# Optimization experiments

Hardware: AMD Instinct MI355X
Metric: run time of the kernel (lower is better)

Reference implementation:

```python
import jax, jax.numpy as jnp
import numpy as np

A0, A1, A2 = 1.0, 1.0, 0.5  # Taylor coefficients of exp around 0 (p=2)

B, H, N, D = 2, 16, 4096, 32


def setup_inputs() -> dict:
    key = jax.random.key(0)
    kq, kk, kv = jax.random.split(key, 3)
    q = jax.random.normal(kq, (B, H, N, D), dtype=jnp.float32)
    k = jax.random.normal(kk, (B, H, N, D), dtype=jnp.float32)
    v = jax.random.normal(kv, (B, H, N, D), dtype=jnp.float32)
    return {"q": q, "k": k, "v": v}


def reference(q, k, v):
    # fastmax_function with p=2, mask=False, normalize=False, dropout=0 -> temperature=1
    b, h, n, d = q.shape
    # quadratic feature maps: flatten of outer products, [b,h,n,d*d]
    q2 = (q[..., :, None] * q[..., None, :]).reshape(b, h, n, d * d)
    k2 = (k[..., :, None] * k[..., None, :]).reshape(b, h, n, d * d)
    # numerator: a0*sum(v) + a1*q(k^T v) + a2*q2(k2^T v)
    second_term = A1 * jnp.einsum('bhnd,bhne->bhde', k, v)           # [b,h,d,d]
    third_term = A2 * jnp.einsum('bhnf,bhne->bhfe', k2, v)           # [b,h,d^2,d]
    ans = (jnp.einsum('bhnd,bhde->bhne', q, second_term)
           + jnp.einsum('bhnf,bhfe->bhne', q2, third_term)
           + A0 * jnp.sum(v, axis=-2, keepdims=True))                 # [b,h,n,d]
    # denominator: a0*n + a1*q.sum(k) + a2*q2.sum(k2)
    div = (A0 * n
           + A1 * jnp.einsum('bhnd,bhd->bhn', q, jnp.sum(k, axis=-2))
           + A2 * jnp.einsum('bhnf,bhf->bhn', q2, jnp.sum(k2, axis=-2)))  # [b,h,n]
    return ans / div[..., None]
```

## Files before the change

### kernel.cpp

```cpp
#include <hip/hip_runtime.h>

#define NTOK 4096
#define NBH  32
#define NF   576
#define NE   33
#define NKT  18
#define GTF_BH (NKT * 3 * 64 * 8)
#define GTF_HALF (9 * 3 * 64 * 8)
#define KC   16
#define NSTG 2
#define NVB  (KC * NBH)
#define NP8  (NBH * NE * NF / 8)

typedef _Float16 half_t;
typedef _Float16 half8 __attribute__((ext_vector_type(8)));
typedef _Float16 half4v __attribute__((ext_vector_type(4)));
typedef float f32x4 __attribute__((ext_vector_type(4)));
typedef unsigned int u32;

#define MFMA16(A,B,C) __builtin_amdgcn_mfma_f32_16x16x32_f16((A),(B),(C),0,0,0)

#define ASYNC_CP16(dst_lds, src_glb) \
    __builtin_amdgcn_global_load_lds( \
        (const __attribute__((address_space(1))) u32*)(const void*)(src_glb), \
        (__attribute__((address_space(3))) u32*)(void*)(dst_lds), 16, 0, 0)

static __device__ __forceinline__ half8 splat8(half_t x) {
    return (half8){x, x, x, x, x, x, x, x};
}

static __device__ __forceinline__ int FS(int d) { return (d + (d >> 3)) & 15; }

__global__ __launch_bounds__(256, 2)
void ta_kernel(const float* __restrict__ kin, const float* __restrict__ vin,
               half_t* __restrict__ P)
{
    __shared__ __align__(16) half_t kb0[2 * 4096];
    __shared__ __align__(16) half_t vb0[2 * 4096];

    const int vb = blockIdx.x;
    const int bh = vb & (NBH - 1), kc = vb >> 5;
    const int t = threadIdx.x;
    const int w = t >> 6, lane = t & 63, l16 = lane & 15, quad = lane >> 4;
    const int pw = w * 144;
    const half8 h05 = splat8((half_t)0.5f);

    f32x4 acc[9][3];
    #pragma unroll
    for (int m = 0; m < 9; ++m)
        #pragma unroll
        for (int e = 0; e < 3; ++e)
            acc[m][e] = (f32x4){0.f, 0.f, 0.f, 0.f};

    int rotoff[9], rotsalt[9];
    #pragma unroll
    for (int mt = 0; mt < 9; ++mt) {
        const int pm = pw + mt * 16;
        int ro = 0, rs = 0;
        if (pm >= 32 && pm < 512) {
            const int s  = 1 + ((pm - 32) >> 5);
            const int i0 = (pm - 32) & 31;
            const int r  = (i0 + l16 + s) & 31;
            ro = r * 128;
            rs = FS(r);
        }
        rotoff[mt] = ro;
        rotsalt[mt] = rs;
    }
    const int sh0 = FS(l16), sh1 = FS(l16 + 16);

    const size_t fbase = ((size_t)bh * NTOK + kc * 256) * 32;
    const float4* k4 = (const float4*)kin + fbase / 4;
    const float4* v4 = (const float4*)vin + fbase / 4;

    float kaf[16], vaf[16];
    auto loadst = [&](int s) {
        const int base = s * 1024;
        #pragma unroll
        for (int r = 0; r < 4; ++r) {
            float4 kk = k4[base + t + 256 * r];
            float4 vv = v4[base + t + 256 * r];
            kaf[4*r+0] = kk.x; kaf[4*r+1] = kk.y; kaf[4*r+2] = kk.z; kaf[4*r+3] = kk.w;
            vaf[4*r+0] = vv.x; vaf[4*r+1] = vv.y; vaf[4*r+2] = vv.z; vaf[4*r+3] = vv.w;
        }
    };
    auto writest = [&](int buf) {
        half_t* kb = kb0 + buf * 4096;
        half_t* vb2 = vb0 + buf * 4096;
        #pragma unroll
        for (int r = 0; r < 4; ++r) {
            const int fi = t + 256 * r;
            const int n = fi >> 3, d4 = fi & 7;
            const int c = n >> 3, j = n & 7;
            #pragma unroll
            for (int i = 0; i < 4; ++i) {
                const int d = 4 * d4 + i;
                const int a = d * 128 + ((c ^ FS(d)) << 3) + j;
                kb[a] = (half_t)kaf[4*r+i];
                vb2[a] = (half_t)vaf[4*r+i];
            }
        }
    };
    auto compute = [&](int buf) {
        const half_t* kb = kb0 + buf * 4096;
        const half_t* vbp = vb0 + buf * 4096;
        #pragma unroll 1
        for (int kk = 0; kk < 4; ++kk) {
            const int c = kk * 4 + quad;
            half8 kj0 = *(const half8*)&kb[l16 * 128 + ((c ^ sh0) << 3)];
            half8 kj1 = *(const half8*)&kb[(l16 + 16) * 128 + ((c ^ sh1) << 3)];
            half8 bf0 = *(const half8*)&vbp[l16 * 128 + ((c ^ sh0) << 3)];
            half8 bf1 = *(const half8*)&vbp[(l16 + 16) * 128 + ((c ^ sh1) << 3)];
            half_t onec = (l16 == 0) ? (half_t)1 : (half_t)0;
            half8 bf2 = splat8(onec);
            #pragma unroll
            for (int mt = 0; mt < 9; ++mt) {
                const int pm = pw + mt * 16;
                half8 af;
                if (pm < 32) {
                    af = pm ? kj1 : kj0;
                } else if (pm < 512) {
                    half8 rot = *(const half8*)&kb[rotoff[mt] + ((c ^ rotsalt[mt]) << 3)];
                    af = (((pm - 32) & 16) ? kj1 : kj0) * rot;
                } else if (pm == 512) {
                    af = kj0 * kj1;
                } else if (pm == 528) {
                    af = (kj0 * h05) * kj0;
                } else if (pm == 544) {
                    af = (kj1 * h05) * kj1;
                } else {
                    af = bf2;
                }
                acc[mt][0] = MFMA16(af, bf0, acc[mt][0]);
                acc[mt][1] = MFMA16(af, bf1, acc[mt][1]);
                acc[mt][2] = MFMA16(af, bf2, acc[mt][2]);
            }
        }
    };

    loadst(0);
    writest(0);
    __syncthreads();
    #pragma unroll 1
    for (int st = 0; st < NSTG; ++st) {
        const int cur = st & 1;
        if (st + 1 < NSTG) loadst(st + 1);
        compute(cur);
        if (st + 1 < NSTG) { writest(cur ^ 1); __syncthreads(); }
    }

    half_t* Pb = P + ((size_t)kc * NBH + bh) * NE * NF;
    #pragma unroll
    for (int mt = 0; mt < 9; ++mt) {
        int p0 = pw + mt * 16 + quad * 4;
        half4v h0 = {(half_t)acc[mt][0][0], (half_t)acc[mt][0][1],
                     (half_t)acc[mt][0][2], (half_t)acc[mt][0][3]};
        half4v h1 = {(half_t)acc[mt][1][0], (half_t)acc[mt][1][1],
                     (half_t)acc[mt][1][2], (half_t)acc[mt][1][3]};
        *(half4v*)&Pb[(size_t)l16 * NF + p0] = h0;
        *(half4v*)&Pb[(size_t)(l16 + 16) * NF + p0] = h1;
        if (l16 == 0) {
            half4v h2 = {(half_t)acc[mt][2][0], (half_t)acc[mt][2][1],
                         (half_t)acc[mt][2][2], (half_t)acc[mt][2][3]};
            *(half4v*)&Pb[(size_t)32 * NF + p0] = h2;
        }
    }
}

__global__ __launch_bounds__(256)
void ar_kernel(const half_t* __restrict__ P, half_t* __restrict__ GtF)
{
    const int idx = blockIdx.x * 256 + threadIdx.x;
    if (idx >= NP8) return;
    float s[8] = {0.f, 0.f, 0.f, 0.f, 0.f, 0.f, 0.f, 0.f};
    for (int c = 0; c < KC; ++c) {
        half8 h = *(const half8*)&P[(size_t)c * (NBH * NE * NF) + (size_t)idx * 8];
        #pragma unroll
        for (int j = 0; j < 8; ++j) s[j] += (float)h[j];
    }
    half8 o;
    #pragma unroll
    for (int j = 0; j < 8; ++j) o[j] = (half_t)s[j];
    int row = idx / 72;
    int p8 = idx - row * 72;
    int e = row % 33, bhh = row / 33;
    int kt = p8 >> 2, quad = p8 & 3;
    int rr = e >> 4, l16 = e & 15;
    size_t dst8 = (size_t)bhh * (GTF_BH / 8)
                + (size_t)(kt * 3 + rr) * 64 + quad * 16 + l16;
    *(half8*)&GtF[dst8 * 8] = o;
}

__global__ __launch_bounds__(256)
void b_kernel(const float* __restrict__ qin, const half_t* __restrict__ GtF,
              float* __restrict__ out)
{
    const int bh = blockIdx.x, mbq = blockIdx.y;
    const int t = threadIdx.x, w = t >> 6, lane = t & 63;
    const int l16 = lane & 15, quad = lane >> 4;
    __shared__ __align__(16) half_t qs2[256 * 56];
    __shared__ __align__(16) half_t gs[GTF_HALF];
    __shared__ float denl[256];
    const size_t nbase = (size_t)bh * NTOK + mbq * 256;

    const half_t* Gsrc = GtF + (size_t)bh * GTF_BH + (size_t)lane * 8;
    auto stage = [&](int phase) {
        const half_t* src = Gsrc + phase * GTF_HALF;
        #pragma unroll
        for (int i = 0; i < 7; ++i) {
            const int c = w + 4 * i;
            if (c < 27)
                ASYNC_CP16(gs + c * 512, src + c * 512);
        }
    };
    stage(0);

    const float4* q4 = (const float4*)(qin + nbase * 32);
    #pragma unroll
    for (int r = 0; r < 8; ++r) {
        int f4 = t + 256 * r, n = f4 >> 3, d4 = f4 & 7;
        float4 vv = q4[f4];
        half4v h = {(half_t)vv.x, (half_t)vv.y, (half_t)vv.z, (half_t)vv.w};
        *(half4v*)&qs2[n * 56 + d4 * 4] = h;
        if (d4 < 4) *(half4v*)&qs2[n * 56 + 32 + d4 * 4] = h;
    }
    __syncthreads();

    const int rbase = w * 64;
    int tb[4];
    #pragma unroll
    for (int mt = 0; mt < 4; ++mt) tb[mt] = (rbase + mt * 16 + l16) * 56;

    half8 vq[4], hv[4], gv[4];
    #pragma unroll
    for (int mt = 0; mt < 4; ++mt) {
        const int qb = tb[mt] + quad * 8;
        vq[mt] = *(const half8*)&qs2[qb];
        hv[mt] = *(const half8*)&qs2[qb + 8];
        gv[mt] = *(const half8*)&qs2[qb + 16];
    }

    f32x4 acc[3][4];
    #pragma unroll
    for (int a = 0; a < 3; ++a)
        #pragma unroll
        for (int b = 0; b < 4; ++b)
            acc[a][b] = (f32x4){0.f, 0.f, 0.f, 0.f};

#define LDB(ktL, B) do { \
    _Pragma("unroll") \
    for (int rr = 0; rr < 3; ++rr) \
        (B)[rr] = *(const half8*)&gs[(((ktL) * 3 + rr) * 64 + lane) * 8]; \
} while (0)

#define DO_MFMA(AF, B) do { \
    _Pragma("unroll") \
    for (int mt = 0; mt < 4; ++mt) { \
        acc[0][mt] = MFMA16((AF)[mt], (B)[0], acc[0][mt]); \
        acc[1][mt] = MFMA16((AF)[mt], (B)[1], acc[1][mt]); \
        acc[2][mt] = MFMA16((AF)[mt], (B)[2], acc[2][mt]); \
    } \
} while (0)

#define QCHUNK(S, KTL) do { \
    half8 Bc[3]; \
    LDB((KTL), Bc); \
    half8 af[4]; \
    _Pragma("unroll") \
    for (int mt = 0; mt < 4; ++mt) { \
        half8 lo = ((S) < 8) ? vq[mt] : hv[mt]; \
        half8 hi = ((S) < 8) ? hv[mt] : gv[mt]; \
        half8 rot = __builtin_shufflevector(lo, hi, \
            ((S) & 7) + 0, ((S) & 7) + 1, ((S) & 7) + 2, ((S) & 7) + 3, \
            ((S) & 7) + 4, ((S) & 7) + 5, ((S) & 7) + 6, ((S) & 7) + 7); \
        af[mt] = vq[mt] * rot; \
    } \
    DO_MFMA(af, Bc); \
} while (0)

    {
        half8 Bc[3];
        LDB(0, Bc);
        DO_MFMA(vq, Bc);
    }
    QCHUNK(1, 1);  QCHUNK(2, 2);  QCHUNK(3, 3);  QCHUNK(4, 4);
    QCHUNK(5, 5);  QCHUNK(6, 6);  QCHUNK(7, 7);  QCHUNK(8, 8);

    __syncthreads();
    stage(1);
    __syncthreads();

    QCHUNK(9, 0);  QCHUNK(10, 1); QCHUNK(11, 2); QCHUNK(12, 3);
    QCHUNK(13, 4); QCHUNK(14, 5); QCHUNK(15, 6);

    {
        half8 Bc[3];
        LDB(7, Bc);
        half8 af[4];
        #pragma unroll
        for (int mt = 0; mt < 4; ++mt) {
            const int off = tb[mt] + ((quad >= 2) ? (quad - 2) : quad) * 8;
            half8 Ld = *(const half8*)&qs2[off];
            af[mt] = (quad < 2) ? (vq[mt] * gv[mt]) : (Ld * Ld);
        }
        DO_MFMA(af, Bc);
    }
    {
        half8 Bc[3];
        LDB(8, Bc);
        const half8 zero = {};
        half8 c10 = {};
        c10[0] = (half_t)1;
        half8 af[4];
        #pragma unroll
        for (int mt = 0; mt < 4; ++mt) {
            half8 d = gv[mt] * gv[mt];
            af[mt] = (quad < 2) ? d : ((quad == 2) ? c10 : zero);
        }
        DO_MFMA(af, Bc);
    }
#undef QCHUNK
#undef DO_MFMA
#undef LDB

    if (l16 == 0) {
        #pragma unroll
        for (int mt = 0; mt < 4; ++mt)
            #pragma unroll
            for (int r = 0; r < 4; ++r)
                denl[rbase + mt * 16 + quad * 4 + r] = acc[2][mt][r];
    }
    __syncthreads();
    #pragma unroll
    for (int mt = 0; mt < 4; ++mt) {
        float inv[4];
        #pragma unroll
        for (int r = 0; r < 4; ++r)
            inv[r] = __builtin_amdgcn_rcpf(denl[rbase + mt * 16 + quad * 4 + r]);
        #pragma unroll
        for (int r = 0; r < 4; ++r) {
            size_t ro = (nbase + rbase + mt * 16 + quad * 4 + r) * 32;
            out[ro + l16] = acc[0][mt][r] * inv[r];
            out[ro + l16 + 16] = acc[1][mt][r] * inv[r];
        }
    }
}

extern "C" void kernel_launch(void* const* d_in, const int* in_sizes, int n_in,
                              void* d_out, int out_size, void* d_ws, size_t ws_size,
                              hipStream_t stream)
{
    const float* q = (const float*)d_in[0];
    const float* k = (const float*)d_in[1];
    const float* v = (const float*)d_in[2];
    float* out = (float*)d_out;

    const size_t planeHalves = (size_t)NBH * NE * NF;
    half_t* P = (half_t*)d_ws;
    half_t* GtF = P + (size_t)KC * planeHalves;

    ta_kernel<<<dim3(NVB), 256, 0, stream>>>(k, v, P);
    ar_kernel<<<dim3((NP8 + 255) / 256), 256, 0, stream>>>(P, GtF);
    b_kernel<<<dim3(NBH, 16), 256, 0, stream>>>(q, GtF, out);
}
```

Measured before the change: 118.8 us.

## Split token chunks finer and drop double-buffered staging in first-pass kernel

The number of token chunks per head doubles (KC 16 to 32), so each block handles 128 tokens in a single stage. The two-stage double-buffered LDS pipeline goes away, which halves shared memory, and launch bounds rise so four blocks can occupy a CU. The intent is more blocks and higher occupancy to hide load latency instead of software pipelining. In exchange there are twice as many partial results to write and reduce in the later pass, which adds global traffic.

New measurement: 176.2 us. +48.4%, slower.

```diff
diff --git a/kernel.cpp b/kernel.cpp
--- a/kernel.cpp
+++ b/kernel.cpp
@@ -7,8 +7,7 @@
 #define NKT  18
 #define GTF_BH (NKT * 3 * 64 * 8)
 #define GTF_HALF (9 * 3 * 64 * 8)
-#define KC   16
-#define NSTG 2
+#define KC   32
 #define NVB  (KC * NBH)
 #define NP8  (NBH * NE * NF / 8)
 
@@ -31,12 +30,12 @@
 
 static __device__ __forceinline__ int FS(int d) { return (d + (d >> 3)) & 15; }
 
-__global__ __launch_bounds__(256, 2)
+__global__ __launch_bounds__(256, 4)
 void ta_kernel(const float* __restrict__ kin, const float* __restrict__ vin,
                half_t* __restrict__ P)
 {
-    __shared__ __align__(16) half_t kb0[2 * 4096];
-    __shared__ __align__(16) half_t vb0[2 * 4096];
+    __shared__ __align__(16) half_t kb0[4096];
+    __shared__ __align__(16) half_t vb0[4096];
 
     const int vb = blockIdx.x;
     const int bh = vb & (NBH - 1), kc = vb >> 5;
@@ -69,84 +68,64 @@
     }
     const int sh0 = FS(l16), sh1 = FS(l16 + 16);
 
-    const size_t fbase = ((size_t)bh * NTOK + kc * 256) * 32;
+    const size_t fbase = ((size_t)bh * NTOK + kc * 128) * 32;
     const float4* k4 = (const float4*)kin + fbase / 4;
     const float4* v4 = (const float4*)vin + fbase / 4;
 
     float kaf[16], vaf[16];
-    auto loadst = [&](int s) {
-        const int base = s * 1024;
-        #pragma unroll
-        for (int r = 0; r < 4; ++r) {
-            float4 kk = k4[base + t + 256 * r];
-            float4 vv = v4[base + t + 256 * r];
-            kaf[4*r+0] = kk.x; kaf[4*r+1] = kk.y; kaf[4*r+2] = kk.z; kaf[4*r+3] = kk.w;
-            vaf[4*r+0] = vv.x; vaf[4*r+1] = vv.y; vaf[4*r+2] = vv.z; vaf[4*r+3] = vv.w;
-        }
-    };
-    auto writest = [&](int buf) {
-        half_t* kb = kb0 + buf * 4096;
-        half_t* vb2 = vb0 + buf * 4096;
-        #pragma unroll
-        for (int r = 0; r < 4; ++r) {
-            const int fi = t + 256 * r;
-            const int n = fi >> 3, d4 = fi & 7;
-            const int c = n >> 3, j = n & 7;
-            #pragma unroll
-            for (int i = 0; i < 4; ++i) {
-                const int d = 4 * d4 + i;
-                const int a = d * 128 + ((c ^ FS(d)) << 3) + j;
-                kb[a] = (half_t)kaf[4*r+i];
-                vb2[a] = (half_t)vaf[4*r+i];
+    #pragma unroll
+    for (int r = 0; r < 4; ++r) {
+        float4 kk = k4[t + 256 * r];
+        float4 vv = v4[t + 256 * r];
+        kaf[4*r+0] = kk.x; kaf[4*r+1] = kk.y; kaf[4*r+2] = kk.z; kaf[4*r+3] = kk.w;
+        vaf[4*r+0] = vv.x; vaf[4*r+1] = vv.y; vaf[4*r+2] = vv.z; vaf[4*r+3] = vv.w;
+    }
+    #pragma unroll
+    for (int r = 0; r < 4; ++r) {
+        const int fi = t + 256 * r;
+        const int n = fi >> 3, d4 = fi & 7;
+        const int c = n >> 3, j = n & 7;
+        #pragma unroll
+        for (int i = 0; i < 4; ++i) {
+            const int d = 4 * d4 + i;
+            const int a = d * 128 + ((c ^ FS(d)) << 3) + j;
+            kb0[a] = (half_t)kaf[4*r+i];
+            vb0[a] = (half_t)vaf[4*r+i];
+        }
+    }
+    __syncthreads();
+
+    #pragma unroll 1
+    for (int kk = 0; kk < 4; ++kk) {
+        const int c = kk * 4 + quad;
+        half8 kj0 = *(const half8*)&kb0[l16 * 128 + ((c ^ sh0) << 3)];
+        half8 kj1 = *(const half8*)&kb0[(l16 + 16) * 128 + ((c ^ sh1) << 3)];
+        half8 bf0 = *(const half8*)&vb0[l16 * 128 + ((c ^ sh0) << 3)];
+        half8 bf1 = *(const half8*)&vb0[(l16 + 16) * 128 + ((c ^ sh1) << 3)];
+        half_t onec = (l16 == 0) ? (half_t)1 : (half_t)0;
+        half8 bf2 = splat8(onec);
+        #pragma unroll
+        for (int mt = 0; mt < 9; ++mt) {
+            const int pm = pw + mt * 16;
+            half8 af;
+            if (pm < 32) {
+                af = pm ? kj1 : kj0;
+            } else if (pm < 512) {
+                half8 rot = *(const half8*)&kb0[rotoff[mt] + ((c ^ rotsalt[mt]) << 3)];
+                af = (((pm - 32) & 16) ? kj1 : kj0) * rot;
+            } else if (pm == 512) {
+                af = kj0 * kj1;
+            } else if (pm == 528) {
+                af = (kj0 * h05) * kj0;
+            } else if (pm == 544) {
+                af = (kj1 * h05) * kj1;
+            } else {
+                af = bf2;
             }
-        }
-    };
-    auto compute = [&](int buf) {
-        const half_t* kb = kb0 + buf * 4096;
-        const half_t* vbp = vb0 + buf * 4096;
-        #pragma unroll 1
-        for (int kk = 0; kk < 4; ++kk) {
-            const int c = kk * 4 + quad;
-            half8 kj0 = *(const half8*)&kb[l16 * 128 + ((c ^ sh0) << 3)];
-            half8 kj1 = *(const half8*)&kb[(l16 + 16) * 128 + ((c ^ sh1) << 3)];
-            half8 bf0 = *(const half8*)&vbp[l16 * 128 + ((c ^ sh0) << 3)];
-            half8 bf1 = *(const half8*)&vbp[(l16 + 16) * 128 + ((c ^ sh1) << 3)];
-            half_t onec = (l16 == 0) ? (half_t)1 : (half_t)0;
-            half8 bf2 = splat8(onec);
-            #pragma unroll
-            for (int mt = 0; mt < 9; ++mt) {
-                const int pm = pw + mt * 16;
-                half8 af;
-                if (pm < 32) {
-                    af = pm ? kj1 : kj0;
-                } else if (pm < 512) {
-                    half8 rot = *(const half8*)&kb[rotoff[mt] + ((c ^ rotsalt[mt]) << 3)];
-                    af = (((pm - 32) & 16) ? kj1 : kj0) * rot;
-                } else if (pm == 512) {
-                    af = kj0 * kj1;
-                } else if (pm == 528) {
-                    af = (kj0 * h05) * kj0;
-                } else if (pm == 544) {
-                    af = (kj1 * h05) * kj1;
-                } else {
-                    af = bf2;
-                }
-                acc[mt][0] = MFMA16(af, bf0, acc[mt][0]);
-                acc[mt][1] = MFMA16(af, bf1, acc[mt][1]);
-                acc[mt][2] = MFMA16(af, bf2, acc[mt][2]);
-            }
-        }
-    };
-
-    loadst(0);
-    writest(0);
-    __syncthreads();
-    #pragma unroll 1
-    for (int st = 0; st < NSTG; ++st) {
-        const int cur = st & 1;
-        if (st + 1 < NSTG) loadst(st + 1);
-        compute(cur);
-        if (st + 1 < NSTG) { writest(cur ^ 1); __syncthreads(); }
+            acc[mt][0] = MFMA16(af, bf0, acc[mt][0]);
+            acc[mt][1] = MFMA16(af, bf1, acc[mt][1]);
+            acc[mt][2] = MFMA16(af, bf2, acc[mt][2]);
+        }
     }
 
     half_t* Pb = P + ((size_t)kc * NBH + bh) * NE * NF;
```
